# Performance work log

Measured on AMD Instinct MI355X. Metric: run time of the kernel, lower is better.

Reference implementation:

```python
import jax, jax.numpy as jnp
import numpy as np

N = 100000          # nodes
C_IN = 128          # incoming clusters (mask columns)
F = 116             # n_feature (e.g. AAL atlas ROIs)
N_CLUSTER = 64      # output clusters
EPS_BN = 1e-5
EPS_CORR = 1e-12


def setup_inputs() -> dict:
    key = jax.random.key(0)
    ks = jax.random.split(key, 8)
    inp = {
        "x_cov": jax.random.normal(ks[0], (N, F, F), dtype=jnp.float32),
        "mask_labels": jax.random.randint(ks[1], (N,), 0, C_IN, dtype=jnp.int32),
        "gumbel_u": jax.random.uniform(ks[2], (C_IN, N_CLUSTER), dtype=jnp.float32),
        "w1": jax.random.normal(ks[3], (256, F), dtype=jnp.float32) / np.sqrt(F),
        "b1": jnp.zeros((256,), dtype=jnp.float32),
        "g1": jnp.ones((F,), dtype=jnp.float32),
        "be1": jnp.zeros((F,), dtype=jnp.float32),
        "w2": jax.random.normal(ks[4], (N_CLUSTER, 256), dtype=jnp.float32) / np.sqrt(256.0),
        "b2": jnp.zeros((N_CLUSTER,), dtype=jnp.float32),
        "g2": jnp.ones((256,), dtype=jnp.float32),
        "be2": jnp.zeros((256,), dtype=jnp.float32),
    }
    return inp


def _batch_norm(x, g, b):
    # BatchNorm1d in training mode: batch stats, biased variance
    mu = x.mean(axis=0)
    var = x.var(axis=0)
    return g * (x - mu) * jax.lax.rsqrt(var + EPS_BN) + b


def _correlation_readout(cov):
    # cov: [C, F, F] -> correlation matrix, then row-mean readout -> [C, F]
    d = jnp.sqrt(jnp.clip(jnp.diagonal(cov, axis1=1, axis2=2), 0.0))  # [C, F]
    corr = cov / (d[:, :, None] * d[:, None, :] + EPS_CORR)
    return corr.mean(axis=-1)


def reference(x_cov, mask_labels, gumbel_u, w1, b1, g1, be1, w2, b2, g2, be2):
    # sparse.mm(mask.T, x_cov.reshape(-1, F*F)) == segment-sum of node covs per cluster
    flat = x_cov.reshape(-1, F * F)                                   # [N, F*F]
    cov = jax.ops.segment_sum(flat, mask_labels, num_segments=C_IN)   # [C_in, F*F]
    cov = cov.reshape(-1, F, F)                                       # [C_in, F, F]

    x_corr = _correlation_readout(cov)                                # [C_in, F]

    # MLP: bn -> lin -> relu -> bn -> lin
    h = jax.nn.relu(_batch_norm(x_corr, g1, be1) @ w1.T + b1)         # [C_in, 256]
    logits = _batch_norm(h, g2, be2) @ w2.T + b2                      # [C_in, n_cluster]

    # hard gumbel-softmax, tau=1, dim=1, straight-through
    u = jnp.clip(gumbel_u, 1e-6, 1.0 - 1e-6)
    gumbels = -jnp.log(-jnp.log(u))
    y_soft = jax.nn.softmax(logits + gumbels, axis=1)
    y_hard = jax.nn.one_hot(jnp.argmax(y_soft, axis=1), N_CLUSTER, dtype=y_soft.dtype)
    mask_out = y_hard - jax.lax.stop_gradient(y_soft) + y_soft        # [C_in, n_cluster]

    return cov, x_corr, mask_out
```

## Files before the change

kernel.cpp:

```cpp
#include <hip/hip_runtime.h>

#define N_NODES 100000
#define C_IN    128
#define F       116
#define FF      (F * F)
#define H1      256
#define NCL     64
#define EPS_BN   1e-5f
#define EPS_CORR 1e-12f


__global__ __launch_bounds__(256) void k_hist(const int* __restrict__ lab,
                                              int* __restrict__ cnt) {
    __shared__ int lh[C_IN];
    int t = threadIdx.x;
    if (t < C_IN) lh[t] = 0;
    __syncthreads();
    for (int n = blockIdx.x * blockDim.x + t; n < N_NODES; n += gridDim.x * blockDim.x)
        atomicAdd(&lh[lab[n]], 1);
    __syncthreads();
    if (t < C_IN) {
        int v = lh[t];
        if (v) atomicAdd(&cnt[t], v);
    }
}

__global__ __launch_bounds__(128) void k_prefix(const int* __restrict__ cnt,
                                                int* __restrict__ coff,
                                                int* __restrict__ cursor) {
    __shared__ int s[C_IN];
    int t = threadIdx.x;
    int mine = cnt[t];
    s[t] = mine;
    __syncthreads();
    for (int d = 1; d < C_IN; d <<= 1) {
        int v = (t >= d) ? s[t - d] : 0;
        __syncthreads();
        s[t] += v;
        __syncthreads();
    }
    int excl = s[t] - mine;
    coff[t] = excl;
    cursor[t * 8] = excl;
    if (t == C_IN - 1) coff[C_IN] = s[t];
}

__global__ __launch_bounds__(256) void k_scatter(const int* __restrict__ lab,
                                                 int* __restrict__ cursor,
                                                 int* __restrict__ bucket) {
    int stride = gridDim.x * blockDim.x;
    for (int n = blockIdx.x * blockDim.x + threadIdx.x; n < N_NODES; n += stride) {
        int l = lab[n];
        int pos = atomicAdd(&cursor[l * 8], 1);
        bucket[pos] = n;
    }
}


__global__ __launch_bounds__(256) void k_segsum(const float* __restrict__ x,
                                                const int* __restrict__ bucket,
                                                const int* __restrict__ coff,
                                                float* __restrict__ cov) {
    const int label = blockIdx.y;
    const int col   = blockIdx.x * 256 + threadIdx.x;
    const bool valid = col < (FF / 4);
    const int j4 = (valid ? col : (FF / 4 - 1)) * 4;

    const int beg = coff[label];
    const int end = coff[label + 1];

    __shared__ int nd[256];
    float4 acc = make_float4(0.f, 0.f, 0.f, 0.f);

    for (int base = beg; base < end; base += 256) {
        int cl = end - base;
        if (cl > 256) cl = 256;
        __syncthreads();
        if (threadIdx.x < cl) nd[threadIdx.x] = bucket[base + threadIdx.x];
        __syncthreads();

        int i = 0;
        for (; i + 4 <= cl; i += 4) {
            int n0 = nd[i], n1 = nd[i + 1], n2 = nd[i + 2], n3 = nd[i + 3];
            float4 a0 = *(const float4*)(x + (size_t)n0 * FF + j4);
            float4 a1 = *(const float4*)(x + (size_t)n1 * FF + j4);
            float4 a2 = *(const float4*)(x + (size_t)n2 * FF + j4);
            float4 a3 = *(const float4*)(x + (size_t)n3 * FF + j4);
            acc.x += a0.x; acc.y += a0.y; acc.z += a0.z; acc.w += a0.w;
            acc.x += a1.x; acc.y += a1.y; acc.z += a1.z; acc.w += a1.w;
            acc.x += a2.x; acc.y += a2.y; acc.z += a2.z; acc.w += a2.w;
            acc.x += a3.x; acc.y += a3.y; acc.z += a3.z; acc.w += a3.w;
        }
        for (; i < cl; ++i) {
            float4 a = *(const float4*)(x + (size_t)nd[i] * FF + j4);
            acc.x += a.x; acc.y += a.y; acc.z += a.z; acc.w += a.w;
        }
    }

    if (valid)
        *(float4*)(cov + (size_t)label * FF + j4) = acc;
}


__global__ __launch_bounds__(128) void k_corr(const float* __restrict__ cov,
                                              float* __restrict__ xcorr) {
    const int c = blockIdx.x;
    const float* Cm = cov + (size_t)c * FF;
    __shared__ float d[F];
    int t = threadIdx.x;
    if (t < F) {
        float dg = Cm[t * F + t];
        d[t] = sqrtf(fmaxf(dg, 0.f));
    }
    __syncthreads();
    if (t < F) {
        float di = d[t];
        float s = 0.f;
        for (int j = 0; j < F; ++j)
            s += Cm[t * F + j] / (di * d[j] + EPS_CORR);
        xcorr[c * F + t] = s / (float)F;
    }
}


__global__ __launch_bounds__(128) void k_stats1(const float* __restrict__ xcorr,
                                                float* __restrict__ mu,
                                                float* __restrict__ rs) {
    int f = threadIdx.x;
    if (f >= F) return;
    float s = 0.f;
    for (int c = 0; c < C_IN; ++c) s += xcorr[c * F + f];
    float m = s / (float)C_IN;
    float v = 0.f;
    for (int c = 0; c < C_IN; ++c) {
        float dd = xcorr[c * F + f] - m;
        v += dd * dd;
    }
    v /= (float)C_IN;
    mu[f] = m;
    rs[f] = rsqrtf(v + EPS_BN);
}

__global__ __launch_bounds__(256) void k_mm1(const float* __restrict__ xcorr,
                                             const float* __restrict__ mu1,
                                             const float* __restrict__ rs1,
                                             const float* __restrict__ g1,
                                             const float* __restrict__ be1,
                                             const float* __restrict__ w1,
                                             const float* __restrict__ b1,
                                             float* __restrict__ h) {
    const int c = blockIdx.x;
    __shared__ float xb[F];
    int t = threadIdx.x;
    if (t < F) xb[t] = g1[t] * (xcorr[c * F + t] - mu1[t]) * rs1[t] + be1[t];
    __syncthreads();
    float acc = b1[t];
    const float* wr = w1 + t * F;
    for (int f = 0; f < F; ++f) acc += xb[f] * wr[f];
    h[c * H1 + t] = fmaxf(acc, 0.f);
}

__global__ __launch_bounds__(256) void k_stats2(const float* __restrict__ h,
                                                float* __restrict__ mu,
                                                float* __restrict__ rs) {
    int o = threadIdx.x;
    float s = 0.f;
    for (int c = 0; c < C_IN; ++c) s += h[c * H1 + o];
    float m = s / (float)C_IN;
    float v = 0.f;
    for (int c = 0; c < C_IN; ++c) {
        float dd = h[c * H1 + o] - m;
        v += dd * dd;
    }
    v /= (float)C_IN;
    mu[o] = m;
    rs[o] = rsqrtf(v + EPS_BN);
}

__global__ __launch_bounds__(64) void k_mm2(const float* __restrict__ h,
                                            const float* __restrict__ mu2,
                                            const float* __restrict__ rs2,
                                            const float* __restrict__ g2,
                                            const float* __restrict__ be2,
                                            const float* __restrict__ w2,
                                            const float* __restrict__ b2,
                                            const float* __restrict__ gu,
                                            float* __restrict__ mask) {
    const int c = blockIdx.x;
    const int k = threadIdx.x;
    __shared__ float hb[H1];
    for (int o = k; o < H1; o += 64)
        hb[o] = g2[o] * (h[c * H1 + o] - mu2[o]) * rs2[o] + be2[o];
    __syncthreads();

    float acc = b2[k];
    const float* wr = w2 + k * H1;
    for (int o = 0; o < H1; ++o) acc += hb[o] * wr[o];

    float u = gu[c * NCL + k];
    u = fminf(fmaxf(u, 1e-6f), 1.f - 1e-6f);
    float z = acc - logf(-logf(u));

    float m = z;
    for (int d = 32; d; d >>= 1) m = fmaxf(m, __shfl_xor(m, d));
    float e = expf(z - m);
    float s = e;
    for (int d = 32; d; d >>= 1) s += __shfl_xor(s, d);
    float y = e / s;

    float bv = z; int bi = k;
    for (int d = 32; d; d >>= 1) {
        float ov = __shfl_xor(bv, d);
        int   oi = __shfl_xor(bi, d);
        if (ov > bv || (ov == bv && oi < bi)) { bv = ov; bi = oi; }
    }
    float hard = (k == bi) ? 1.f : 0.f;
    mask[c * NCL + k] = (hard - y) + y;
}


extern "C" void kernel_launch(void* const* d_in, const int* in_sizes, int n_in,
                              void* d_out, int out_size, void* d_ws, size_t ws_size,
                              hipStream_t stream) {
    const float* x_cov = (const float*)d_in[0];
    const int*   lab   = (const int*)d_in[1];
    const float* gu    = (const float*)d_in[2];
    const float* w1    = (const float*)d_in[3];
    const float* b1    = (const float*)d_in[4];
    const float* g1    = (const float*)d_in[5];
    const float* be1   = (const float*)d_in[6];
    const float* w2    = (const float*)d_in[7];
    const float* b2    = (const float*)d_in[8];
    const float* g2    = (const float*)d_in[9];
    const float* be2   = (const float*)d_in[10];

    float* cov_out   = (float*)d_out;
    float* xcorr_out = cov_out + (size_t)C_IN * FF;
    float* mask_out  = xcorr_out + (size_t)C_IN * F;

    int* bucket = (int*)d_ws;
    int* cnt    = bucket + 100000;
    int* coff   = cnt + 128;
    int* cursor = coff + 132;
    float* h    = (float*)(cursor + 1024);
    float* mu1  = h + C_IN * H1;
    float* rs1  = mu1 + 128;
    float* mu2  = rs1 + 128;
    float* rs2  = mu2 + 256;

    hipMemsetAsync(cnt, 0, C_IN * sizeof(int), stream);

    k_hist   <<<128, 256, 0, stream>>>(lab, cnt);
    k_prefix <<<1, 128, 0, stream>>>(cnt, coff, cursor);
    k_scatter<<<256, 256, 0, stream>>>(lab, cursor, bucket);

    k_segsum <<<dim3(14, C_IN), 256, 0, stream>>>(x_cov, bucket, coff, cov_out);

    k_corr   <<<C_IN, 128, 0, stream>>>(cov_out, xcorr_out);

    k_stats1 <<<1, 128, 0, stream>>>(xcorr_out, mu1, rs1);
    k_mm1    <<<C_IN, 256, 0, stream>>>(xcorr_out, mu1, rs1, g1, be1, w1, b1, h);
    k_stats2 <<<1, 256, 0, stream>>>(h, mu2, rs2);
    k_mm2    <<<C_IN, 64, 0, stream>>>(h, mu2, rs2, g2, be2, w2, b2, gu, mask_out);
}
```

Baseline: 990.8 us.

## Use per-block histograms, precomputed offsets, fused BN stats, and split accumulators

Replaces global-atomic histogram and cursor scatter with per-block histograms, a serial block scan, and shared-memory local cursors, which drops the memset and the global atomics. The bucket now stores the node's element offset instead of its index, removing a multiply in the segment-sum gather. The segment sum stages 1024 indices at a time and alternates between two accumulators. The BatchNorm statistic kernels are fused into the matmul kernels, so each block recomputes the column statistics redundantly, and mm2 splits its dot product across 256 threads. The dominant cost is still the 690 MB gather read, so the overall gain is likely small.

Result: faster. 966.5 us (-2.5%).

```diff
diff --git a/kernel.cpp b/kernel.cpp
--- a/kernel.cpp
+++ b/kernel.cpp
@@ -9,56 +9,68 @@
 #define EPS_BN   1e-5f
 #define EPS_CORR 1e-12f
 
+#define NBLK 256
+#define NPB  ((N_NODES + NBLK - 1) / NBLK)
+
 
 __global__ __launch_bounds__(256) void k_hist(const int* __restrict__ lab,
-                                              int* __restrict__ cnt) {
+                                              int* __restrict__ blkhist) {
     __shared__ int lh[C_IN];
-    int t = threadIdx.x;
+    const int b = blockIdx.x, t = threadIdx.x;
     if (t < C_IN) lh[t] = 0;
     __syncthreads();
-    for (int n = blockIdx.x * blockDim.x + t; n < N_NODES; n += gridDim.x * blockDim.x)
+    const int s = b * NPB;
+    int e = s + NPB; if (e > N_NODES) e = N_NODES;
+    for (int n = s + t; n < e; n += 256)
         atomicAdd(&lh[lab[n]], 1);
     __syncthreads();
-    if (t < C_IN) {
-        int v = lh[t];
-        if (v) atomicAdd(&cnt[t], v);
-    }
-}
-
-__global__ __launch_bounds__(128) void k_prefix(const int* __restrict__ cnt,
-                                                int* __restrict__ coff,
-                                                int* __restrict__ cursor) {
-    __shared__ int s[C_IN];
-    int t = threadIdx.x;
-    int mine = cnt[t];
-    s[t] = mine;
+    if (t < C_IN) blkhist[b * C_IN + t] = lh[t];
+}
+
+__global__ __launch_bounds__(128) void k_scan(const int* __restrict__ blkhist,
+                                              int* __restrict__ blkoff,
+                                              int* __restrict__ coff) {
+    __shared__ int tot[C_IN];
+    const int l = threadIdx.x;
+    int run = 0;
+    for (int b = 0; b < NBLK; ++b) {
+        int v = blkhist[b * C_IN + l];
+        blkoff[b * C_IN + l] = run;
+        run += v;
+    }
+    const int mine = run;
+    tot[l] = run;
     __syncthreads();
     for (int d = 1; d < C_IN; d <<= 1) {
-        int v = (t >= d) ? s[t - d] : 0;
-        __syncthreads();
-        s[t] += v;
-        __syncthreads();
-    }
-    int excl = s[t] - mine;
-    coff[t] = excl;
-    cursor[t * 8] = excl;
-    if (t == C_IN - 1) coff[C_IN] = s[t];
+        int v = (l >= d) ? tot[l - d] : 0;
+        __syncthreads();
+        tot[l] += v;
+        __syncthreads();
+    }
+    coff[l] = tot[l] - mine;
+    if (l == C_IN - 1) coff[C_IN] = tot[l];
 }
 
 __global__ __launch_bounds__(256) void k_scatter(const int* __restrict__ lab,
-                                                 int* __restrict__ cursor,
-                                                 int* __restrict__ bucket) {
-    int stride = gridDim.x * blockDim.x;
-    for (int n = blockIdx.x * blockDim.x + threadIdx.x; n < N_NODES; n += stride) {
+                                                 const int* __restrict__ blkoff,
+                                                 const int* __restrict__ coff,
+                                                 unsigned* __restrict__ bucket) {
+    __shared__ int cur[C_IN];
+    const int b = blockIdx.x, t = threadIdx.x;
+    if (t < C_IN) cur[t] = coff[t] + blkoff[b * C_IN + t];
+    __syncthreads();
+    const int s = b * NPB;
+    int e = s + NPB; if (e > N_NODES) e = N_NODES;
+    for (int n = s + t; n < e; n += 256) {
         int l = lab[n];
-        int pos = atomicAdd(&cursor[l * 8], 1);
-        bucket[pos] = n;
+        int pos = atomicAdd(&cur[l], 1);
+        bucket[pos] = (unsigned)n * (unsigned)FF;
     }
 }
 
 
 __global__ __launch_bounds__(256) void k_segsum(const float* __restrict__ x,
-                                                const int* __restrict__ bucket,
+                                                const unsigned* __restrict__ bucket,
                                                 const int* __restrict__ coff,
                                                 float* __restrict__ cov) {
     const int label = blockIdx.y;
@@ -69,36 +81,41 @@
     const int beg = coff[label];
     const int end = coff[label + 1];
 
-    __shared__ int nd[256];
-    float4 acc = make_float4(0.f, 0.f, 0.f, 0.f);
-
-    for (int base = beg; base < end; base += 256) {
+    __shared__ unsigned nd[1024];
+    float4 a0acc = make_float4(0.f, 0.f, 0.f, 0.f);
+    float4 a1acc = make_float4(0.f, 0.f, 0.f, 0.f);
+
+    for (int base = beg; base < end; base += 1024) {
         int cl = end - base;
-        if (cl > 256) cl = 256;
-        __syncthreads();
-        if (threadIdx.x < cl) nd[threadIdx.x] = bucket[base + threadIdx.x];
+        if (cl > 1024) cl = 1024;
+        __syncthreads();
+        for (int i = threadIdx.x; i < cl; i += 256)
+            nd[i] = bucket[base + i];
         __syncthreads();
 
         int i = 0;
         for (; i + 4 <= cl; i += 4) {
-            int n0 = nd[i], n1 = nd[i + 1], n2 = nd[i + 2], n3 = nd[i + 3];
-            float4 a0 = *(const float4*)(x + (size_t)n0 * FF + j4);
-            float4 a1 = *(const float4*)(x + (size_t)n1 * FF + j4);
-            float4 a2 = *(const float4*)(x + (size_t)n2 * FF + j4);
-            float4 a3 = *(const float4*)(x + (size_t)n3 * FF + j4);
-            acc.x += a0.x; acc.y += a0.y; acc.z += a0.z; acc.w += a0.w;
-            acc.x += a1.x; acc.y += a1.y; acc.z += a1.z; acc.w += a1.w;
-            acc.x += a2.x; acc.y += a2.y; acc.z += a2.z; acc.w += a2.w;
-            acc.x += a3.x; acc.y += a3.y; acc.z += a3.z; acc.w += a3.w;
+            const float4 v0 = *(const float4*)(x + (size_t)nd[i]     + j4);
+            const float4 v1 = *(const float4*)(x + (size_t)nd[i + 1] + j4);
+            const float4 v2 = *(const float4*)(x + (size_t)nd[i + 2] + j4);
+            const float4 v3 = *(const float4*)(x + (size_t)nd[i + 3] + j4);
+            a0acc.x += v0.x; a0acc.y += v0.y; a0acc.z += v0.z; a0acc.w += v0.w;
+            a1acc.x += v1.x; a1acc.y += v1.y; a1acc.z += v1.z; a1acc.w += v1.w;
+            a0acc.x += v2.x; a0acc.y += v2.y; a0acc.z += v2.z; a0acc.w += v2.w;
+            a1acc.x += v3.x; a1acc.y += v3.y; a1acc.z += v3.z; a1acc.w += v3.w;
         }
         for (; i < cl; ++i) {
-            float4 a = *(const float4*)(x + (size_t)nd[i] * FF + j4);
-            acc.x += a.x; acc.y += a.y; acc.z += a.z; acc.w += a.w;
-        }
-    }
-
-    if (valid)
-        *(float4*)(cov + (size_t)label * FF + j4) = acc;
+            const float4 v = *(const float4*)(x + (size_t)nd[i] + j4);
+            a0acc.x += v.x; a0acc.y += v.y; a0acc.z += v.z; a0acc.w += v.w;
+        }
+    }
+
+    if (valid) {
+        float4 r;
+        r.x = a0acc.x + a1acc.x; r.y = a0acc.y + a1acc.y;
+        r.z = a0acc.z + a1acc.z; r.w = a0acc.w + a1acc.w;
+        *(float4*)(cov + (size_t)label * FF + j4) = r;
+    }
 }
 
 
@@ -107,14 +124,11 @@
     const int c = blockIdx.x;
     const float* Cm = cov + (size_t)c * FF;
     __shared__ float d[F];
-    int t = threadIdx.x;
+    const int t = threadIdx.x;
+    if (t < F) d[t] = sqrtf(fmaxf(Cm[t * F + t], 0.f));
+    __syncthreads();
     if (t < F) {
-        float dg = Cm[t * F + t];
-        d[t] = sqrtf(fmaxf(dg, 0.f));
-    }
-    __syncthreads();
-    if (t < F) {
-        float di = d[t];
+        const float di = d[t];
         float s = 0.f;
         for (int j = 0; j < F; ++j)
             s += Cm[t * F + j] / (di * d[j] + EPS_CORR);
@@ -123,36 +137,27 @@
 }
 
 
-__global__ __launch_bounds__(128) void k_stats1(const float* __restrict__ xcorr,
-                                                float* __restrict__ mu,
-                                                float* __restrict__ rs) {
-    int f = threadIdx.x;
-    if (f >= F) return;
-    float s = 0.f;
-    for (int c = 0; c < C_IN; ++c) s += xcorr[c * F + f];
-    float m = s / (float)C_IN;
-    float v = 0.f;
-    for (int c = 0; c < C_IN; ++c) {
-        float dd = xcorr[c * F + f] - m;
-        v += dd * dd;
-    }
-    v /= (float)C_IN;
-    mu[f] = m;
-    rs[f] = rsqrtf(v + EPS_BN);
-}
-
 __global__ __launch_bounds__(256) void k_mm1(const float* __restrict__ xcorr,
-                                             const float* __restrict__ mu1,
-                                             const float* __restrict__ rs1,
                                              const float* __restrict__ g1,
                                              const float* __restrict__ be1,
                                              const float* __restrict__ w1,
                                              const float* __restrict__ b1,
                                              float* __restrict__ h) {
     const int c = blockIdx.x;
+    const int t = threadIdx.x;
     __shared__ float xb[F];
-    int t = threadIdx.x;
-    if (t < F) xb[t] = g1[t] * (xcorr[c * F + t] - mu1[t]) * rs1[t] + be1[t];
+    if (t < F) {
+        float s = 0.f;
+        for (int cc = 0; cc < C_IN; ++cc) s += xcorr[cc * F + t];
+        const float m = s / (float)C_IN;
+        float v = 0.f;
+        for (int cc = 0; cc < C_IN; ++cc) {
+            const float dd = xcorr[cc * F + t] - m;
+            v += dd * dd;
+        }
+        v /= (float)C_IN;
+        xb[t] = g1[t] * (xcorr[c * F + t] - m) * rsqrtf(v + EPS_BN) + be1[t];
+    }
     __syncthreads();
     float acc = b1[t];
     const float* wr = w1 + t * F;
@@ -160,62 +165,62 @@
     h[c * H1 + t] = fmaxf(acc, 0.f);
 }
 
-__global__ __launch_bounds__(256) void k_stats2(const float* __restrict__ h,
-                                                float* __restrict__ mu,
-                                                float* __restrict__ rs) {
-    int o = threadIdx.x;
-    float s = 0.f;
-    for (int c = 0; c < C_IN; ++c) s += h[c * H1 + o];
-    float m = s / (float)C_IN;
-    float v = 0.f;
-    for (int c = 0; c < C_IN; ++c) {
-        float dd = h[c * H1 + o] - m;
-        v += dd * dd;
-    }
-    v /= (float)C_IN;
-    mu[o] = m;
-    rs[o] = rsqrtf(v + EPS_BN);
-}
-
-__global__ __launch_bounds__(64) void k_mm2(const float* __restrict__ h,
-                                            const float* __restrict__ mu2,
-                                            const float* __restrict__ rs2,
-                                            const float* __restrict__ g2,
-                                            const float* __restrict__ be2,
-                                            const float* __restrict__ w2,
-                                            const float* __restrict__ b2,
-                                            const float* __restrict__ gu,
-                                            float* __restrict__ mask) {
+__global__ __launch_bounds__(256) void k_mm2(const float* __restrict__ h,
+                                             const float* __restrict__ g2,
+                                             const float* __restrict__ be2,
+                                             const float* __restrict__ w2,
+                                             const float* __restrict__ b2,
+                                             const float* __restrict__ gu,
+                                             float* __restrict__ mask) {
     const int c = blockIdx.x;
-    const int k = threadIdx.x;
+    const int t = threadIdx.x;
     __shared__ float hb[H1];
-    for (int o = k; o < H1; o += 64)
-        hb[o] = g2[o] * (h[c * H1 + o] - mu2[o]) * rs2[o] + be2[o];
-    __syncthreads();
-
-    float acc = b2[k];
-    const float* wr = w2 + k * H1;
-    for (int o = 0; o < H1; ++o) acc += hb[o] * wr[o];
-
-    float u = gu[c * NCL + k];
-    u = fminf(fmaxf(u, 1e-6f), 1.f - 1e-6f);
-    float z = acc - logf(-logf(u));
-
-    float m = z;
-    for (int d = 32; d; d >>= 1) m = fmaxf(m, __shfl_xor(m, d));
-    float e = expf(z - m);
-    float s = e;
-    for (int d = 32; d; d >>= 1) s += __shfl_xor(s, d);
-    float y = e / s;
-
-    float bv = z; int bi = k;
-    for (int d = 32; d; d >>= 1) {
-        float ov = __shfl_xor(bv, d);
-        int   oi = __shfl_xor(bi, d);
-        if (ov > bv || (ov == bv && oi < bi)) { bv = ov; bi = oi; }
-    }
-    float hard = (k == bi) ? 1.f : 0.f;
-    mask[c * NCL + k] = (hard - y) + y;
+    __shared__ float part[4][NCL];
+
+    {
+        float s = 0.f;
+        for (int cc = 0; cc < C_IN; ++cc) s += h[cc * H1 + t];
+        const float m = s / (float)C_IN;
+        float v = 0.f;
+        for (int cc = 0; cc < C_IN; ++cc) {
+            const float dd = h[cc * H1 + t] - m;
+            v += dd * dd;
+        }
+        v /= (float)C_IN;
+        hb[t] = g2[t] * (h[c * H1 + t] - m) * rsqrtf(v + EPS_BN) + be2[t];
+    }
+    __syncthreads();
+
+    const int k = t & 63, p = t >> 6;
+    float acc = 0.f;
+    const float* wr = w2 + k * H1 + p * 64;
+    const float* hp = hb + p * 64;
+    for (int o = 0; o < 64; ++o) acc += hp[o] * wr[o];
+    part[p][k] = acc;
+    __syncthreads();
+
+    if (t < NCL) {
+        float z = b2[t] + part[0][t] + part[1][t] + part[2][t] + part[3][t];
+        float u = gu[c * NCL + t];
+        u = fminf(fmaxf(u, 1e-6f), 1.f - 1e-6f);
+        z = z - logf(-logf(u));
+
+        float m = z;
+        for (int d = 32; d; d >>= 1) m = fmaxf(m, __shfl_xor(m, d));
+        const float e = expf(z - m);
+        float s = e;
+        for (int d = 32; d; d >>= 1) s += __shfl_xor(s, d);
+        const float y = e / s;
+
+        float bv = z; int bi = t;
+        for (int d = 32; d; d >>= 1) {
+            float ov = __shfl_xor(bv, d);
+            int   oi = __shfl_xor(bi, d);
+            if (ov > bv || (ov == bv && oi < bi)) { bv = ov; bi = oi; }
+        }
+        const float hard = (t == bi) ? 1.f : 0.f;
+        mask[c * NCL + t] = (hard - y) + y;
+    }
 }
 
 
@@ -238,28 +243,19 @@
     float* xcorr_out = cov_out + (size_t)C_IN * FF;
     float* mask_out  = xcorr_out + (size_t)C_IN * F;
 
-    int* bucket = (int*)d_ws;
-    int* cnt    = bucket + 100000;
-    int* coff   = cnt + 128;
-    int* cursor = coff + 132;
-    float* h    = (float*)(cursor + 1024);
-    float* mu1  = h + C_IN * H1;
-    float* rs1  = mu1 + 128;
-    float* mu2  = rs1 + 128;
-    float* rs2  = mu2 + 256;
-
-    hipMemsetAsync(cnt, 0, C_IN * sizeof(int), stream);
-
-    k_hist   <<<128, 256, 0, stream>>>(lab, cnt);
-    k_prefix <<<1, 128, 0, stream>>>(cnt, coff, cursor);
-    k_scatter<<<256, 256, 0, stream>>>(lab, cursor, bucket);
+    int*      blkhist = (int*)d_ws;
+    int*      blkoff  = blkhist + NBLK * C_IN;
+    int*      coff    = blkoff + NBLK * C_IN;
+    unsigned* bucket  = (unsigned*)(coff + 132);
+    float*    h       = (float*)(bucket + N_NODES);
+
+    k_hist   <<<NBLK, 256, 0, stream>>>(lab, blkhist);
+    k_scan   <<<1, 128, 0, stream>>>(blkhist, blkoff, coff);
+    k_scatter<<<NBLK, 256, 0, stream>>>(lab, blkoff, coff, bucket);
 
     k_segsum <<<dim3(14, C_IN), 256, 0, stream>>>(x_cov, bucket, coff, cov_out);
 
     k_corr   <<<C_IN, 128, 0, stream>>>(cov_out, xcorr_out);
-
-    k_stats1 <<<1, 128, 0, stream>>>(xcorr_out, mu1, rs1);
-    k_mm1    <<<C_IN, 256, 0, stream>>>(xcorr_out, mu1, rs1, g1, be1, w1, b1, h);
-    k_stats2 <<<1, 256, 0, stream>>>(h, mu2, rs2);
-    k_mm2    <<<C_IN, 64, 0, stream>>>(h, mu2, rs2, g2, be2, w2, b2, gu, mask_out);
-}
+    k_mm1    <<<C_IN, 256, 0, stream>>>(xcorr_out, g1, be1, w1, b1, h);
+    k_mm2    <<<C_IN, 256, 0, stream>>>(h, g2, be2, w2, b2, gu, mask_out);
+}
```
